# Optimization experiments

Measured on AMD Instinct MI355X. Metric: run time of the kernel, lower is better.

## Reference

```python
import jax, jax.numpy as jnp
import numpy as np

HEADS = 8
HEAD_DIM = 64
FOLD = 2   # fold_w == fold_h
PROP = 2   # proposal_w == proposal_h -> M = PROP*PROP centers
DIM = 512


def _conv1x1(x, w, b):
    # x: [B,C,H,W], w: [O,C] (1x1 conv kernel squeezed), b: [O]
    return jnp.einsum('bchw,oc->bohw', x, w) + b[None, :, None, None]


def _normalize(x):
    # F.normalize along last dim (eps-clamped L2 norm)
    n = jnp.linalg.norm(x, axis=-1, keepdims=True)
    return x / jnp.maximum(n, 1e-12)


def _fold(t, f):
    # 'b c (f1 w) (f2 h) -> (b f1 f2) c w h'
    b, c, W, H = t.shape
    return t.reshape(b, c, f, W // f, f, H // f).transpose(0, 2, 4, 1, 3, 5).reshape(b * f * f, c, W // f, H // f)


def _unfold(t, f):
    # '(b f1 f2) c w h -> b c (f1 w) (f2 h)'
    bf, c, w, h = t.shape
    b = bf // (f * f)
    return t.reshape(b, f, f, c, w, h).transpose(0, 3, 1, 4, 2, 5).reshape(b, c, f * w, f * h)


def _pool(t, p):
    # AdaptiveAvgPool2d((p,p)) when spatial dims divisible by p
    b, c, W, H = t.shape
    return t.reshape(b, c, p, W // p, p, H // p).mean(axis=(3, 5))


def reference(x, f_w, f_b, v_w, v_b, proj_w, proj_b, sim_alpha, sim_beta):
    B = x.shape[0]
    value = _conv1x1(x, v_w, v_b)
    feat = _conv1x1(x, f_w, f_b)
    # split heads: 'b (e c) w h -> (b e) c w h'
    feat = feat.reshape(B * HEADS, HEAD_DIM, feat.shape[2], feat.shape[3])
    value = value.reshape(B * HEADS, HEAD_DIM, value.shape[2], value.shape[3])
    feat = _fold(feat, FOLD)
    value = _fold(value, FOLD)
    b, c, w, h = feat.shape

    centers = _pool(feat, PROP)                                   # [b,c,p,p]
    value_centers = _pool(value, PROP).reshape(b, c, -1).transpose(0, 2, 1)  # [b,M,c]
    cflat = centers.reshape(b, c, -1).transpose(0, 2, 1)          # [b,M,c]
    M = cflat.shape[1]
    xflat = feat.reshape(b, c, -1).transpose(0, 2, 1)             # [b,N,c]

    cos = jnp.einsum('bmc,bnc->bmn', _normalize(cflat), _normalize(xflat))
    sim = jax.nn.sigmoid(sim_beta + sim_alpha * cos)              # [b,M,N]

    idx = jnp.argmax(sim, axis=1)                                 # [b,N] hard assignment
    sim_max = jnp.max(sim, axis=1)
    L_Clst = -jnp.mean(sim_max)
    mask = jax.nn.one_hot(idx, M, dtype=sim.dtype).transpose(0, 2, 1)  # [b,M,N]
    L_Sep = jnp.mean(jnp.max(sim * (1.0 - mask), axis=1))
    Cn = _normalize(cflat)
    G = jnp.einsum('bmc,bkc->bmk', Cn, Cn)
    L_Orth = jnp.mean((G - jnp.eye(M, dtype=G.dtype)) ** 2)

    sim_m = sim * mask
    vflat = value.reshape(b, c, -1).transpose(0, 2, 1)            # [b,N,c]
    # scatter_sum of values into their assigned cluster == one-hot matmul
    agg = jnp.einsum('bmn,bnc->bmc', mask, vflat)                 # [b,M,c]
    counts = mask.sum(axis=-1, keepdims=True)                     # [b,M,1]
    out = (agg + value_centers) / (counts + 1.0)                  # [b,M,c]
    # masked weighted broadcast back to points (avoids [b,M,N,c] intermediate)
    outp = jnp.einsum('bmn,bmc->bnc', sim_m, out)                 # [b,N,c]
    outp = outp.transpose(0, 2, 1).reshape(b, c, w, h)
    outp = _unfold(outp, FOLD)
    outp = outp.reshape(B, HEADS * HEAD_DIM, outp.shape[2], outp.shape[3])
    outp = _conv1x1(outp, proj_w, proj_b)
    return outp, jnp.stack([L_Orth, L_Clst, L_Sep])


def setup_inputs():
    key = jax.random.key(0)
    ks = jax.random.split(key, 4)
    E = HEADS * HEAD_DIM  # 512
    return {
        'x': jax.random.normal(ks[0], (32, DIM, 32, 32), jnp.float32),
        'f_w': jax.random.normal(ks[1], (E, DIM), jnp.float32) * 0.02,
        'f_b': jnp.zeros((E,), jnp.float32),
        'v_w': jax.random.normal(ks[2], (E, DIM), jnp.float32) * 0.02,
        'v_b': jnp.zeros((E,), jnp.float32),
        'proj_w': jax.random.normal(ks[3], (DIM, E), jnp.float32) * 0.02,
        'proj_b': jnp.zeros((DIM,), jnp.float32),
        'sim_alpha': jnp.ones((1,), jnp.float32),
        'sim_beta': jnp.zeros((1,), jnp.float32),
    }
```

## Files before the change

### kernel.cpp

```cpp
#include <hip/hip_runtime.h>


#define HW 1024

typedef _Float16 f16x8 __attribute__((ext_vector_type(8)));
typedef float f32x4 __attribute__((ext_vector_type(4)));

union H4 { uint2 u; _Float16 h[4]; };
union H8 { uint4 u; _Float16 h[8]; };
union H2 { unsigned int u; _Float16 h[2]; };
union F4 { float4 v; float f[4]; };

__device__ __forceinline__ void gld16(const _Float16* g, _Float16* l) {
    __builtin_amdgcn_global_load_lds(
        (const __attribute__((address_space(1))) void*)g,
        (__attribute__((address_space(3))) void*)l, 16, 0, 0);
}

__global__ __launch_bounds__(256) void k_wsplit(
    const float* __restrict__ fw, const float* __restrict__ vw,
    _Float16* __restrict__ fwh, _Float16* __restrict__ fwl,
    _Float16* __restrict__ vwh)
{
    const int i = (blockIdx.x * 256 + threadIdx.x) * 4;
    F4 a;
    a.v = *(const float4*)&fw[i];
    H4 h, l;
#pragma unroll
    for (int j = 0; j < 4; ++j) {
        const float s = a.f[j] * 256.f;
        h.h[j] = (_Float16)s;
        l.h[j] = (_Float16)(s - (float)h.h[j]);
    }
    *(uint2*)&fwh[i] = h.u;
    *(uint2*)&fwl[i] = l.u;
    a.v = *(const float4*)&vw[i];
#pragma unroll
    for (int j = 0; j < 4; ++j) h.h[j] = (_Float16)(a.f[j] * 256.f);
    *(uint2*)&vwh[i] = h.u;
}

__global__ __launch_bounds__(256) void k_xsplit(
    const float* __restrict__ x,
    _Float16* __restrict__ xh, _Float16* __restrict__ xl)
{
    __shared__ float tile[64][65];
    const int t = threadIdx.x;
    const int b = blockIdx.z;
    const int k0 = blockIdx.y * 64;
    const int n0 = blockIdx.x * 64;
    const float* Xb = x + (size_t)b * (512 * HW);

#pragma unroll
    for (int j = 0; j < 16; ++j) {
        const int k = j * 4 + (t >> 6);
        const int n = t & 63;
        tile[k][n] = Xb[(size_t)(k0 + k) * HW + n0 + n];
    }
    __syncthreads();
#pragma unroll
    for (int j = 0; j < 8; ++j) {
        const int n = j * 8 + (t >> 5);
        const int kp = t & 31;
        const float s0 = tile[kp * 2][n] * 256.f;
        const float s1 = tile[kp * 2 + 1][n] * 256.f;
        H2 hh, hl;
        hh.h[0] = (_Float16)s0;
        hh.h[1] = (_Float16)s1;
        hl.h[0] = (_Float16)(s0 - (float)hh.h[0]);
        hl.h[1] = (_Float16)(s1 - (float)hh.h[1]);
        const size_t o = ((size_t)b * 1024 + n0 + n) * 512 + k0 + kp * 2;
        *(unsigned int*)&xh[o] = hh.u;
        *(unsigned int*)&xl[o] = hl.u;
    }
}

__global__ __launch_bounds__(256) void k_feat(
    const _Float16* __restrict__ fwh, const _Float16* __restrict__ fwl,
    const float* __restrict__ bias,
    const _Float16* __restrict__ xh, const _Float16* __restrict__ xl,
    float* __restrict__ feat_T, float* __restrict__ centers_f)
{
    __shared__ _Float16 Ah[128 * 32], Al[128 * 32], Bh[128 * 32], Bl[128 * 32];
    __shared__ float pool_lds[2][128][4];
    const int t = threadIdx.x, lane = t & 63, wv = t >> 6;
    const int b = blockIdx.z, o0 = blockIdx.y * 128, p0 = blockIdx.x * 128;
    const int wr = wv >> 1, wc = wv & 1;

    f32x4 acc[4][4];
#pragma unroll
    for (int i = 0; i < 4; ++i)
#pragma unroll
        for (int j = 0; j < 4; ++j) acc[i][j] = (f32x4){0.f, 0.f, 0.f, 0.f};

    const _Float16* ash = fwh + (size_t)(o0 + wv * 32 + (lane >> 2)) * 512 + (lane & 3) * 8;
    const _Float16* asl = fwl + (size_t)(o0 + wv * 32 + (lane >> 2)) * 512 + (lane & 3) * 8;
    const size_t brow = (size_t)b * 1024 + p0 + wv * 32 + (lane >> 2);
    const _Float16* bsh = xh + brow * 512 + (lane & 3) * 8;
    const _Float16* bsl = xl + brow * 512 + (lane & 3) * 8;

    for (int kb = 0; kb < 16; ++kb) {
        const int k0 = kb * 32;
        __syncthreads();
#pragma unroll
        for (int j = 0; j < 2; ++j) {
            gld16(ash + (size_t)(j * 16) * 512 + k0, &Ah[(wv * 32 + j * 16) * 32]);
            gld16(asl + (size_t)(j * 16) * 512 + k0, &Al[(wv * 32 + j * 16) * 32]);
            gld16(bsh + (size_t)(j * 16) * 512 + k0, &Bh[(wv * 32 + j * 16) * 32]);
            gld16(bsl + (size_t)(j * 16) * 512 + k0, &Bl[(wv * 32 + j * 16) * 32]);
        }
        __syncthreads();
        f16x8 ah[4], al[4], bh[4], bl[4];
#pragma unroll
        for (int i = 0; i < 4; ++i) {
            const int ao = (wr * 64 + i * 16 + (lane & 15)) * 32 + (lane >> 4) * 8;
            const int bo = (wc * 64 + i * 16 + (lane & 15)) * 32 + (lane >> 4) * 8;
            ah[i] = *(f16x8*)&Ah[ao];
            al[i] = *(f16x8*)&Al[ao];
            bh[i] = *(f16x8*)&Bh[bo];
            bl[i] = *(f16x8*)&Bl[bo];
        }
#pragma unroll
        for (int mi = 0; mi < 4; ++mi)
#pragma unroll
            for (int nj = 0; nj < 4; ++nj) {
                acc[mi][nj] = __builtin_amdgcn_mfma_f32_16x16x32_f16(ah[mi], bh[nj], acc[mi][nj], 0, 0, 0);
                acc[mi][nj] = __builtin_amdgcn_mfma_f32_16x16x32_f16(ah[mi], bl[nj], acc[mi][nj], 0, 0, 0);
                acc[mi][nj] = __builtin_amdgcn_mfma_f32_16x16x32_f16(al[mi], bh[nj], acc[mi][nj], 0, 0, 0);
            }
    }

    const int pj = (lane >> 3) & 1;
    float ps[16][2];
#pragma unroll
    for (int mi = 0; mi < 4; ++mi) {
        const int obase = o0 + wr * 64 + mi * 16 + (lane >> 4) * 4;
        F4 bs4;
        bs4.v = *(const float4*)&bias[obase];
#pragma unroll
        for (int r = 0; r < 4; ++r) { ps[mi * 4 + r][0] = 0.f; ps[mi * 4 + r][1] = 0.f; }
#pragma unroll
        for (int nj = 0; nj < 4; ++nj) {
            const int p = p0 + wc * 64 + nj * 16 + (lane & 15);
            F4 vv;
#pragma unroll
            for (int r = 0; r < 4; ++r) {
                vv.f[r] = acc[mi][nj][r] * (1.f / 65536.f) + bs4.f[r];
                ps[mi * 4 + r][nj & 1] += vv.f[r];
            }
            *(float4*)&feat_T[((size_t)b * 1024 + p) * 512 + obase] = vv.v;
        }
    }
#pragma unroll
    for (int q = 0; q < 16; ++q)
#pragma unroll
        for (int f2s = 0; f2s < 2; ++f2s) {
            ps[q][f2s] += __shfl_xor(ps[q][f2s], 1);
            ps[q][f2s] += __shfl_xor(ps[q][f2s], 2);
            ps[q][f2s] += __shfl_xor(ps[q][f2s], 4);
        }
    if ((lane & 7) == 0) {
#pragma unroll
        for (int mi = 0; mi < 4; ++mi)
#pragma unroll
            for (int r = 0; r < 4; ++r) {
                const int ol = wr * 64 + mi * 16 + (lane >> 4) * 4 + r;
                pool_lds[wc][ol][0 * 2 + pj] = ps[mi * 4 + r][0];
                pool_lds[wc][ol][1 * 2 + pj] = ps[mi * 4 + r][1];
            }
    }
    __syncthreads();
#pragma unroll
    for (int u = 0; u < 2; ++u) {
        const int idx = u * 256 + t;
        const int g = idx >> 7, o = idx & 127;
        centers_f[(((size_t)b * 8 + blockIdx.x) * 4 + g) * 512 + o0 + o] =
            pool_lds[0][o][g] + pool_lds[1][o][g];
    }
}

__global__ __launch_bounds__(256) void k_value(
    const _Float16* __restrict__ vwh, const float* __restrict__ bias,
    const _Float16* __restrict__ xh,
    _Float16* __restrict__ value_T, float* __restrict__ centers_v)
{
    __shared__ _Float16 Ah[128 * 32], Bh[128 * 32];
    __shared__ float pool_lds[2][128][4];
    const int t = threadIdx.x, lane = t & 63, wv = t >> 6;
    const int b = blockIdx.z, o0 = blockIdx.y * 128, p0 = blockIdx.x * 128;
    const int wr = wv >> 1, wc = wv & 1;

    f32x4 acc[4][4];
#pragma unroll
    for (int i = 0; i < 4; ++i)
#pragma unroll
        for (int j = 0; j < 4; ++j) acc[i][j] = (f32x4){0.f, 0.f, 0.f, 0.f};

    const _Float16* ash = vwh + (size_t)(o0 + wv * 32 + (lane >> 2)) * 512 + (lane & 3) * 8;
    const _Float16* bsh = xh + ((size_t)b * 1024 + p0 + wv * 32 + (lane >> 2)) * 512 + (lane & 3) * 8;

    for (int kb = 0; kb < 16; ++kb) {
        const int k0 = kb * 32;
        __syncthreads();
#pragma unroll
        for (int j = 0; j < 2; ++j) {
            gld16(ash + (size_t)(j * 16) * 512 + k0, &Ah[(wv * 32 + j * 16) * 32]);
            gld16(bsh + (size_t)(j * 16) * 512 + k0, &Bh[(wv * 32 + j * 16) * 32]);
        }
        __syncthreads();
        f16x8 ah[4], bh[4];
#pragma unroll
        for (int i = 0; i < 4; ++i) {
            ah[i] = *(f16x8*)&Ah[(wr * 64 + i * 16 + (lane & 15)) * 32 + (lane >> 4) * 8];
            bh[i] = *(f16x8*)&Bh[(wc * 64 + i * 16 + (lane & 15)) * 32 + (lane >> 4) * 8];
        }
#pragma unroll
        for (int mi = 0; mi < 4; ++mi)
#pragma unroll
            for (int nj = 0; nj < 4; ++nj)
                acc[mi][nj] = __builtin_amdgcn_mfma_f32_16x16x32_f16(ah[mi], bh[nj], acc[mi][nj], 0, 0, 0);
    }

    const int pj = (lane >> 3) & 1;
    float ps[16][2];
#pragma unroll
    for (int mi = 0; mi < 4; ++mi) {
        const int obase = o0 + wr * 64 + mi * 16 + (lane >> 4) * 4;
        F4 bs4;
        bs4.v = *(const float4*)&bias[obase];
#pragma unroll
        for (int r = 0; r < 4; ++r) { ps[mi * 4 + r][0] = 0.f; ps[mi * 4 + r][1] = 0.f; }
#pragma unroll
        for (int nj = 0; nj < 4; ++nj) {
            const int p = p0 + wc * 64 + nj * 16 + (lane & 15);
            H4 hv;
#pragma unroll
            for (int r = 0; r < 4; ++r) {
                const float v = acc[mi][nj][r] * (1.f / 65536.f) + bs4.f[r];
                ps[mi * 4 + r][nj & 1] += v;
                hv.h[r] = (_Float16)v;
            }
            *(uint2*)&value_T[((size_t)b * 1024 + p) * 512 + obase] = hv.u;
        }
    }
#pragma unroll
    for (int q = 0; q < 16; ++q)
#pragma unroll
        for (int f2s = 0; f2s < 2; ++f2s) {
            ps[q][f2s] += __shfl_xor(ps[q][f2s], 1);
            ps[q][f2s] += __shfl_xor(ps[q][f2s], 2);
            ps[q][f2s] += __shfl_xor(ps[q][f2s], 4);
        }
    if ((lane & 7) == 0) {
#pragma unroll
        for (int mi = 0; mi < 4; ++mi)
#pragma unroll
            for (int r = 0; r < 4; ++r) {
                const int ol = wr * 64 + mi * 16 + (lane >> 4) * 4 + r;
                pool_lds[wc][ol][0 * 2 + pj] = ps[mi * 4 + r][0];
                pool_lds[wc][ol][1 * 2 + pj] = ps[mi * 4 + r][1];
            }
    }
    __syncthreads();
#pragma unroll
    for (int u = 0; u < 2; ++u) {
        const int idx = u * 256 + t;
        const int g = idx >> 7, o = idx & 127;
        centers_v[(((size_t)b * 8 + blockIdx.x) * 4 + g) * 512 + o0 + o] =
            pool_lds[0][o][g] + pool_lds[1][o][g];
    }
}

__global__ __launch_bounds__(256) void k_cluster(
    const float* __restrict__ feat_T, const _Float16* __restrict__ value_T,
    const float* __restrict__ centers_f, const float* __restrict__ centers_v,
    const float* __restrict__ alpha_p, const float* __restrict__ beta_p,
    _Float16* __restrict__ outpT, float* __restrict__ part)
{
    __shared__ _Float16 vbuf[256 * 64];
    __shared__ float cnl[4][64];
    __shared__ float vcl[4][64];
    __shared__ float obuf[4][68];
    __shared__ int   sidx[256];
    __shared__ float sbest[256];
    __shared__ float scrt[4][4][64];
    __shared__ int   cntw[4][4];
    __shared__ float red[8];
    __shared__ float gsc[16];

    const int t = threadIdx.x, lane = t & 63, wv = t >> 6;
    const int bp = blockIdx.x;
    const int f2 = bp & 1, f1 = (bp >> 1) & 1, head = (bp >> 2) & 7, b = bp >> 5;

    const int m = wv, cc = lane;
    const int pi = m >> 1, pj = m & 1, g = f2 * 2 + pj;
    const int pt = 4 * f1 + 2 * pi;
    {
        const float* cf = centers_f + (((size_t)b * 8 + pt) * 4 + g) * 512 + head * 64 + cc;
        const float c = (cf[0] + cf[4 * 512]) * (1.f / 64.f);
        float ss = c * c;
#pragma unroll
        for (int off = 32; off > 0; off >>= 1) ss += __shfl_xor(ss, off);
        const float inv = 1.f / fmaxf(sqrtf(ss), 1e-12f);
        cnl[m][cc] = c * inv;
        const float* cv = centers_v + (((size_t)b * 8 + pt) * 4 + g) * 512 + head * 64 + cc;
        vcl[m][cc] = (cv[0] + cv[4 * 512]) * (1.f / 64.f);
    }
    __syncthreads();

    if (t < 16) {
        const int gm = t >> 2, gk = t & 3;
        float gg = 0.f;
        for (int c = 0; c < 64; ++c) gg += cnl[gm][c] * cnl[gk][c];
        const float d = gg - (gm == gk ? 1.f : 0.f);
        gsc[t] = d * d;
    }

    const float alpha = alpha_p[0], beta = beta_p[0];
    const int n = t;
    const int pg = (f1 * 16 + (n >> 4)) * 32 + f2 * 16 + (n & 15);
    const float* fp = feat_T + ((size_t)b * 1024 + pg) * 512 + head * 64;
    float ssf = 0.f, d0 = 0.f, d1 = 0.f, d2 = 0.f, d3 = 0.f;
#pragma unroll
    for (int c4 = 0; c4 < 16; ++c4) {
        F4 fv;
        fv.v = *(const float4*)&fp[c4 * 4];
        const float4 c0 = *(const float4*)&cnl[0][c4 * 4];
        const float4 c1 = *(const float4*)&cnl[1][c4 * 4];
        const float4 c2 = *(const float4*)&cnl[2][c4 * 4];
        const float4 c3 = *(const float4*)&cnl[3][c4 * 4];
        ssf += fv.f[0]*fv.f[0] + fv.f[1]*fv.f[1] + fv.f[2]*fv.f[2] + fv.f[3]*fv.f[3];
        d0 += fv.f[0]*c0.x + fv.f[1]*c0.y + fv.f[2]*c0.z + fv.f[3]*c0.w;
        d1 += fv.f[0]*c1.x + fv.f[1]*c1.y + fv.f[2]*c1.z + fv.f[3]*c1.w;
        d2 += fv.f[0]*c2.x + fv.f[1]*c2.y + fv.f[2]*c2.z + fv.f[3]*c2.w;
        d3 += fv.f[0]*c3.x + fv.f[1]*c3.y + fv.f[2]*c3.z + fv.f[3]*c3.w;
    }
    const float invf = 1.f / fmaxf(sqrtf(ssf), 1e-12f);
    float simv[4];
    simv[0] = d0 * invf;
    simv[1] = d1 * invf;
    simv[2] = d2 * invf;
    simv[3] = d3 * invf;
#pragma unroll
    for (int mm = 0; mm < 4; ++mm)
        simv[mm] = 1.f / (1.f + expf(-(beta + alpha * simv[mm])));
    float best = simv[0], second = -1.f;
    int idx = 0;
#pragma unroll
    for (int mm = 1; mm < 4; ++mm) {
        if (simv[mm] > best) { second = best; best = simv[mm]; idx = mm; }
        else second = fmaxf(second, simv[mm]);
    }
    sidx[n] = idx;
    sbest[n] = best;

    const _Float16* vp = value_T + ((size_t)b * 1024 + pg) * 512 + head * 64;
#pragma unroll
    for (int j = 0; j < 8; ++j) {
        const uint4 v = *(const uint4*)&vp[j * 8];
        *(uint4*)&vbuf[n * 64 + ((j * 8) ^ ((n & 7) << 3))] = v;
    }

    float bsum = best, s2sum = second;
#pragma unroll
    for (int off = 32; off > 0; off >>= 1) {
        bsum += __shfl_xor(bsum, off);
        s2sum += __shfl_xor(s2sum, off);
    }
    if (lane == 0) { red[wv] = bsum; red[4 + wv] = s2sum; }
    __syncthreads();
    if (t == 0) {
        part[bp]        = gsc[0] + gsc[1] + gsc[2] + gsc[3] + gsc[4] + gsc[5] + gsc[6] + gsc[7]
                        + gsc[8] + gsc[9] + gsc[10] + gsc[11] + gsc[12] + gsc[13] + gsc[14] + gsc[15];
        part[1024 + bp] = red[0] + red[1] + red[2] + red[3];
        part[2048 + bp] = red[4] + red[5] + red[6] + red[7];
    }

    {
        float ag0 = 0.f, ag1 = 0.f, ag2 = 0.f, ag3 = 0.f;
        int c0i = 0, c1i = 0, c2i = 0, c3i = 0;
        for (int j = 0; j < 64; ++j) {
            const int nn = wv * 64 + j;
            const int id = sidx[nn];
            const float v = (float)vbuf[nn * 64 + (cc ^ ((nn & 7) << 3))];
            ag0 += (id == 0) ? v : 0.f;  c0i += (id == 0);
            ag1 += (id == 1) ? v : 0.f;  c1i += (id == 1);
            ag2 += (id == 2) ? v : 0.f;  c2i += (id == 2);
            ag3 += (id == 3) ? v : 0.f;  c3i += (id == 3);
        }
        scrt[wv][0][cc] = ag0;
        scrt[wv][1][cc] = ag1;
        scrt[wv][2][cc] = ag2;
        scrt[wv][3][cc] = ag3;
        if (lane == 0) {
            cntw[wv][0] = c0i; cntw[wv][1] = c1i;
            cntw[wv][2] = c2i; cntw[wv][3] = c3i;
        }
    }
    __syncthreads();

    {
        const float a = scrt[0][m][cc] + scrt[1][m][cc] + scrt[2][m][cc] + scrt[3][m][cc];
        const int c = cntw[0][m] + cntw[1][m] + cntw[2][m] + cntw[3][m];
        obuf[m][cc] = (a + vcl[m][cc]) / (float)(c + 1);
    }
    __syncthreads();

    const int cch = (t & 3) * 16;
#pragma unroll
    for (int r = 0; r < 4; ++r) {
        const int nn = r * 64 + (t >> 2);
        const int id = sidx[nn];
        const float bs = sbest[nn];
        const int p = (f1 * 16 + (nn >> 4)) * 32 + f2 * 16 + (nn & 15);
        _Float16* dst = outpT + (((size_t)b * 8 + head) * 1024 + p) * 64 + cch;
        const float4 oa = *(const float4*)&obuf[id][cch];
        const float4 ob = *(const float4*)&obuf[id][cch + 4];
        const float4 oc = *(const float4*)&obuf[id][cch + 8];
        const float4 od = *(const float4*)&obuf[id][cch + 12];
        H8 w0, w1;
        w0.h[0] = (_Float16)(bs * oa.x); w0.h[1] = (_Float16)(bs * oa.y);
        w0.h[2] = (_Float16)(bs * oa.z); w0.h[3] = (_Float16)(bs * oa.w);
        w0.h[4] = (_Float16)(bs * ob.x); w0.h[5] = (_Float16)(bs * ob.y);
        w0.h[6] = (_Float16)(bs * ob.z); w0.h[7] = (_Float16)(bs * ob.w);
        w1.h[0] = (_Float16)(bs * oc.x); w1.h[1] = (_Float16)(bs * oc.y);
        w1.h[2] = (_Float16)(bs * oc.z); w1.h[3] = (_Float16)(bs * oc.w);
        w1.h[4] = (_Float16)(bs * od.x); w1.h[5] = (_Float16)(bs * od.y);
        w1.h[6] = (_Float16)(bs * od.z); w1.h[7] = (_Float16)(bs * od.w);
        *(uint4*)dst = w0.u;
        *(uint4*)(dst + 8) = w1.u;
    }
}

__global__ __launch_bounds__(256) void k_proj(
    const float* __restrict__ w, const float* __restrict__ bias,
    const _Float16* __restrict__ outpT,
    const float* __restrict__ part,
    float* __restrict__ dout)
{
    __shared__ _Float16 Ah[128 * 32], Bh[128 * 32];
    __shared__ float fin[12];
    const int t = threadIdx.x, lane = t & 63, wv = t >> 6;

    if (blockIdx.x == 0 && blockIdx.y == 0 && blockIdx.z == 0) {
        float so = part[t] + part[t + 256] + part[t + 512] + part[t + 768];
        float sc = part[1024 + t] + part[1280 + t] + part[1536 + t] + part[1792 + t];
        float sp = part[2048 + t] + part[2304 + t] + part[2560 + t] + part[2816 + t];
#pragma unroll
        for (int off = 32; off > 0; off >>= 1) {
            so += __shfl_xor(so, off);
            sc += __shfl_xor(sc, off);
            sp += __shfl_xor(sp, off);
        }
        if (lane == 0) { fin[wv] = so; fin[4 + wv] = sc; fin[8 + wv] = sp; }
        __syncthreads();
        if (t == 0) {
            dout[16777216]     = (fin[0] + fin[1] + fin[2] + fin[3]) / 16384.f;
            dout[16777216 + 1] = -(fin[4] + fin[5] + fin[6] + fin[7]) / 262144.f;
            dout[16777216 + 2] = (fin[8] + fin[9] + fin[10] + fin[11]) / 262144.f;
        }
        __syncthreads();
    }

    const int b = blockIdx.z, o0 = blockIdx.y * 128, p0 = blockIdx.x * 128;
    const int wr = wv >> 1, wc = wv & 1;

    f32x4 acc[4][4];
#pragma unroll
    for (int i = 0; i < 4; ++i)
#pragma unroll
        for (int j = 0; j < 4; ++j) acc[i][j] = (f32x4){0.f, 0.f, 0.f, 0.f};

    const int srow = p0 + wv * 32 + (lane >> 2);
    const int scol = (lane & 3) * 8;

    for (int kb = 0; kb < 16; ++kb) {
        const int k0 = kb * 32;
        F4 av[4];
#pragma unroll
        for (int j = 0; j < 4; ++j) {
            const int idx = j * 256 + t, row = idx >> 3, q = idx & 7;
            av[j].v = *(const float4*)&w[(size_t)(o0 + row) * 512 + k0 + q * 4];
        }
        __syncthreads();
#pragma unroll
        for (int j = 0; j < 4; ++j) {
            const int idx = j * 256 + t, row = idx >> 3, q = idx & 7;
            H4 hh;
#pragma unroll
            for (int i = 0; i < 4; ++i) hh.h[i] = (_Float16)(av[j].f[i] * 256.f);
            *(uint2*)&Ah[row * 32 + q * 4] = hh.u;
        }
        const _Float16* bsrc = outpT + (((size_t)b * 8 + (kb >> 1)) * 1024 + srow) * 64
                               + (kb & 1) * 32 + scol;
        gld16(bsrc,            &Bh[(wv * 32) * 32]);
        gld16(bsrc + 16 * 64,  &Bh[(wv * 32 + 16) * 32]);
        __syncthreads();
        f16x8 ah[4], bh[4];
#pragma unroll
        for (int i = 0; i < 4; ++i) {
            ah[i] = *(f16x8*)&Ah[(wr * 64 + i * 16 + (lane & 15)) * 32 + (lane >> 4) * 8];
            bh[i] = *(f16x8*)&Bh[(wc * 64 + i * 16 + (lane & 15)) * 32 + (lane >> 4) * 8];
        }
#pragma unroll
        for (int mi = 0; mi < 4; ++mi)
#pragma unroll
            for (int nj = 0; nj < 4; ++nj)
                acc[mi][nj] = __builtin_amdgcn_mfma_f32_16x16x32_f16(ah[mi], bh[nj], acc[mi][nj], 0, 0, 0);
    }
#pragma unroll
    for (int mi = 0; mi < 4; ++mi)
#pragma unroll
        for (int r = 0; r < 4; ++r) {
            const int o = o0 + wr * 64 + mi * 16 + (lane >> 4) * 4 + r;
            const float bs = bias[o];
#pragma unroll
            for (int nj = 0; nj < 4; ++nj) {
                const int p = p0 + wc * 64 + nj * 16 + (lane & 15);
                dout[((size_t)b * 512 + o) * HW + p] = acc[mi][nj][r] * (1.f / 256.f) + bs;
            }
        }
}

extern "C" void kernel_launch(void* const* d_in, const int* in_sizes, int n_in,
                              void* d_out, int out_size, void* d_ws, size_t ws_size,
                              hipStream_t stream)
{
    const float* x   = (const float*)d_in[0];
    const float* f_w = (const float*)d_in[1];
    const float* f_b = (const float*)d_in[2];
    const float* v_w = (const float*)d_in[3];
    const float* v_b = (const float*)d_in[4];
    const float* p_w = (const float*)d_in[5];
    const float* p_b = (const float*)d_in[6];
    const float* s_a = (const float*)d_in[7];
    const float* s_b = (const float*)d_in[8];
    float* out = (float*)d_out;

    char* ws = (char*)d_ws;
    float*     feat_T  = (float*)ws;
    _Float16*  xh      = (_Float16*)(ws + (size_t)64 * 1024 * 1024);
    _Float16*  xl      = (_Float16*)(ws + (size_t)96 * 1024 * 1024);
    _Float16*  outpT   = xh;
    _Float16*  value_T = xl;
    float*     part    = (float*)(ws + (size_t)128 * 1024 * 1024);

    _Float16* fwh       = (_Float16*)out;
    _Float16* fwl       = (_Float16*)(out + 131072);
    _Float16* vwh       = (_Float16*)(out + 262144);
    float*    centers_f = out + 393216;
    float*    centers_v = out + 917504;

    k_wsplit <<<dim3(256), 256, 0, stream>>>(f_w, v_w, fwh, fwl, vwh);
    k_xsplit <<<dim3(16, 8, 32), 256, 0, stream>>>(x, xh, xl);
    k_feat   <<<dim3(8, 4, 32), 256, 0, stream>>>(fwh, fwl, f_b, xh, xl, feat_T, centers_f);
    k_value  <<<dim3(8, 4, 32), 256, 0, stream>>>(vwh, v_b, xh, value_T, centers_v);
    k_cluster<<<dim3(1024), 256, 0, stream>>>(feat_T, value_T, centers_f, centers_v,
                                              s_a, s_b, outpT, part);
    k_proj   <<<dim3(8, 4, 32), 256, 0, stream>>>(p_w, p_b, outpT, part, out);
}
```

Before: 202.0 us.

## Double-buffer LDS tiles and XOR-swizzle layout in the three GEMM kernels

Converts the feat, value and projection GEMM main loops to double-buffered LDS, so the global-to-LDS loads for the next K-tile are issued while MFMAs run on the current tile. This also cuts the loop to one barrier per iteration. The LDS layout is XOR-swizzled on both the write and read sides to reduce bank conflicts on the f16x8 fragment reads. The cost is twice the shared memory, which may lower occupancy, and more complex index math.

```diff
diff --git a/kernel.cpp b/kernel.cpp
--- a/kernel.cpp
+++ b/kernel.cpp
@@ -81,7 +81,7 @@
     const _Float16* __restrict__ xh, const _Float16* __restrict__ xl,
     float* __restrict__ feat_T, float* __restrict__ centers_f)
 {
-    __shared__ _Float16 Ah[128 * 32], Al[128 * 32], Bh[128 * 32], Bl[128 * 32];
+    __shared__ _Float16 Ah[2][4096], Al[2][4096], Bh[2][4096], Bl[2][4096];
     __shared__ float pool_lds[2][128][4];
     const int t = threadIdx.x, lane = t & 63, wv = t >> 6;
     const int b = blockIdx.z, o0 = blockIdx.y * 128, p0 = blockIdx.x * 128;
@@ -93,42 +93,53 @@
 #pragma unroll
         for (int j = 0; j < 4; ++j) acc[i][j] = (f32x4){0.f, 0.f, 0.f, 0.f};
 
-    const _Float16* ash = fwh + (size_t)(o0 + wv * 32 + (lane >> 2)) * 512 + (lane & 3) * 8;
-    const _Float16* asl = fwl + (size_t)(o0 + wv * 32 + (lane >> 2)) * 512 + (lane & 3) * 8;
+    const int gslot = ((lane & 3) ^ ((lane >> 3) & 3)) * 8;
+    const _Float16* ash = fwh + (size_t)(o0 + wv * 32 + (lane >> 2)) * 512 + gslot;
+    const _Float16* asl = fwl + (size_t)(o0 + wv * 32 + (lane >> 2)) * 512 + gslot;
     const size_t brow = (size_t)b * 1024 + p0 + wv * 32 + (lane >> 2);
-    const _Float16* bsh = xh + brow * 512 + (lane & 3) * 8;
-    const _Float16* bsl = xl + brow * 512 + (lane & 3) * 8;
-
+    const _Float16* bsh = xh + brow * 512 + gslot;
+    const _Float16* bsl = xl + brow * 512 + gslot;
+
+#define STAGE_F(d, k0)                                              \
+    {                                                               \
+        gld16(ash + (k0),        &Ah[(d)][(wv * 32) * 32]);         \
+        gld16(ash + (k0) + 8192, &Ah[(d)][(wv * 32 + 16) * 32]);    \
+        gld16(asl + (k0),        &Al[(d)][(wv * 32) * 32]);         \
+        gld16(asl + (k0) + 8192, &Al[(d)][(wv * 32 + 16) * 32]);    \
+        gld16(bsh + (k0),        &Bh[(d)][(wv * 32) * 32]);         \
+        gld16(bsh + (k0) + 8192, &Bh[(d)][(wv * 32 + 16) * 32]);    \
+        gld16(bsl + (k0),        &Bl[(d)][(wv * 32) * 32]);         \
+        gld16(bsl + (k0) + 8192, &Bl[(d)][(wv * 32 + 16) * 32]);    \
+    }
+
+    STAGE_F(0, 0);
+    __syncthreads();
+    const int slA = ((lane >> 4) ^ ((lane >> 1) & 3)) * 8;
+    int cur = 0;
     for (int kb = 0; kb < 16; ++kb) {
-        const int k0 = kb * 32;
+        if (kb < 15) STAGE_F(cur ^ 1, (kb + 1) * 32);
+        f16x8 ah4[4], al4[4], bh4[4], bl4[4];
+#pragma unroll
+        for (int i = 0; i < 4; ++i) {
+            const int ao = (wr * 64 + i * 16 + (lane & 15)) * 32 + slA;
+            const int bo = (wc * 64 + i * 16 + (lane & 15)) * 32 + slA;
+            ah4[i] = *(f16x8*)&Ah[cur][ao];
+            al4[i] = *(f16x8*)&Al[cur][ao];
+            bh4[i] = *(f16x8*)&Bh[cur][bo];
+            bl4[i] = *(f16x8*)&Bl[cur][bo];
+        }
+#pragma unroll
+        for (int mi = 0; mi < 4; ++mi)
+#pragma unroll
+            for (int nj = 0; nj < 4; ++nj) {
+                acc[mi][nj] = __builtin_amdgcn_mfma_f32_16x16x32_f16(ah4[mi], bh4[nj], acc[mi][nj], 0, 0, 0);
+                acc[mi][nj] = __builtin_amdgcn_mfma_f32_16x16x32_f16(ah4[mi], bl4[nj], acc[mi][nj], 0, 0, 0);
+                acc[mi][nj] = __builtin_amdgcn_mfma_f32_16x16x32_f16(al4[mi], bh4[nj], acc[mi][nj], 0, 0, 0);
+            }
         __syncthreads();
-#pragma unroll
-        for (int j = 0; j < 2; ++j) {
-            gld16(ash + (size_t)(j * 16) * 512 + k0, &Ah[(wv * 32 + j * 16) * 32]);
-            gld16(asl + (size_t)(j * 16) * 512 + k0, &Al[(wv * 32 + j * 16) * 32]);
-            gld16(bsh + (size_t)(j * 16) * 512 + k0, &Bh[(wv * 32 + j * 16) * 32]);
-            gld16(bsl + (size_t)(j * 16) * 512 + k0, &Bl[(wv * 32 + j * 16) * 32]);
-        }
-        __syncthreads();
-        f16x8 ah[4], al[4], bh[4], bl[4];
-#pragma unroll
-        for (int i = 0; i < 4; ++i) {
-            const int ao = (wr * 64 + i * 16 + (lane & 15)) * 32 + (lane >> 4) * 8;
-            const int bo = (wc * 64 + i * 16 + (lane & 15)) * 32 + (lane >> 4) * 8;
-            ah[i] = *(f16x8*)&Ah[ao];
-            al[i] = *(f16x8*)&Al[ao];
-            bh[i] = *(f16x8*)&Bh[bo];
-            bl[i] = *(f16x8*)&Bl[bo];
-        }
-#pragma unroll
-        for (int mi = 0; mi < 4; ++mi)
-#pragma unroll
-            for (int nj = 0; nj < 4; ++nj) {
-                acc[mi][nj] = __builtin_amdgcn_mfma_f32_16x16x32_f16(ah[mi], bh[nj], acc[mi][nj], 0, 0, 0);
-                acc[mi][nj] = __builtin_amdgcn_mfma_f32_16x16x32_f16(ah[mi], bl[nj], acc[mi][nj], 0, 0, 0);
-                acc[mi][nj] = __builtin_amdgcn_mfma_f32_16x16x32_f16(al[mi], bh[nj], acc[mi][nj], 0, 0, 0);
-            }
-    }
+        cur ^= 1;
+    }
+#undef STAGE_F
 
     const int pj = (lane >> 3) & 1;
     float ps[16][2];
@@ -184,7 +195,7 @@
     const _Float16* __restrict__ xh,
     _Float16* __restrict__ value_T, float* __restrict__ centers_v)
 {
-    __shared__ _Float16 Ah[128 * 32], Bh[128 * 32];
+    __shared__ _Float16 Ah[2][4096], Bh[2][4096];
     __shared__ float pool_lds[2][128][4];
     const int t = threadIdx.x, lane = t & 63, wv = t >> 6;
     const int b = blockIdx.z, o0 = blockIdx.y * 128, p0 = blockIdx.x * 128;
@@ -196,30 +207,39 @@
 #pragma unroll
         for (int j = 0; j < 4; ++j) acc[i][j] = (f32x4){0.f, 0.f, 0.f, 0.f};
 
-    const _Float16* ash = vwh + (size_t)(o0 + wv * 32 + (lane >> 2)) * 512 + (lane & 3) * 8;
-    const _Float16* bsh = xh + ((size_t)b * 1024 + p0 + wv * 32 + (lane >> 2)) * 512 + (lane & 3) * 8;
-
+    const int gslot = ((lane & 3) ^ ((lane >> 3) & 3)) * 8;
+    const _Float16* ash = vwh + (size_t)(o0 + wv * 32 + (lane >> 2)) * 512 + gslot;
+    const _Float16* bsh = xh + ((size_t)b * 1024 + p0 + wv * 32 + (lane >> 2)) * 512 + gslot;
+
+#define STAGE_V(d, k0)                                              \
+    {                                                               \
+        gld16(ash + (k0),        &Ah[(d)][(wv * 32) * 32]);         \
+        gld16(ash + (k0) + 8192, &Ah[(d)][(wv * 32 + 16) * 32]);    \
+        gld16(bsh + (k0),        &Bh[(d)][(wv * 32) * 32]);         \
+        gld16(bsh + (k0) + 8192, &Bh[(d)][(wv * 32 + 16) * 32]);    \
+    }
+
+    STAGE_V(0, 0);
+    __syncthreads();
+    const int slA = ((lane >> 4) ^ ((lane >> 1) & 3)) * 8;
+    int cur = 0;
     for (int kb = 0; kb < 16; ++kb) {
-        const int k0 = kb * 32;
+        if (kb < 15) STAGE_V(cur ^ 1, (kb + 1) * 32);
+        f16x8 ah4[4], bh4[4];
+#pragma unroll
+        for (int i = 0; i < 4; ++i) {
+            ah4[i] = *(f16x8*)&Ah[cur][(wr * 64 + i * 16 + (lane & 15)) * 32 + slA];
+            bh4[i] = *(f16x8*)&Bh[cur][(wc * 64 + i * 16 + (lane & 15)) * 32 + slA];
+        }
+#pragma unroll
+        for (int mi = 0; mi < 4; ++mi)
+#pragma unroll
+            for (int nj = 0; nj < 4; ++nj)
+                acc[mi][nj] = __builtin_amdgcn_mfma_f32_16x16x32_f16(ah4[mi], bh4[nj], acc[mi][nj], 0, 0, 0);
         __syncthreads();
-#pragma unroll
-        for (int j = 0; j < 2; ++j) {
-            gld16(ash + (size_t)(j * 16) * 512 + k0, &Ah[(wv * 32 + j * 16) * 32]);
-            gld16(bsh + (size_t)(j * 16) * 512 + k0, &Bh[(wv * 32 + j * 16) * 32]);
-        }
-        __syncthreads();
-        f16x8 ah[4], bh[4];
-#pragma unroll
-        for (int i = 0; i < 4; ++i) {
-            ah[i] = *(f16x8*)&Ah[(wr * 64 + i * 16 + (lane & 15)) * 32 + (lane >> 4) * 8];
-            bh[i] = *(f16x8*)&Bh[(wc * 64 + i * 16 + (lane & 15)) * 32 + (lane >> 4) * 8];
-        }
-#pragma unroll
-        for (int mi = 0; mi < 4; ++mi)
-#pragma unroll
-            for (int nj = 0; nj < 4; ++nj)
-                acc[mi][nj] = __builtin_amdgcn_mfma_f32_16x16x32_f16(ah[mi], bh[nj], acc[mi][nj], 0, 0, 0);
-    }
+        cur ^= 1;
+    }
+#undef STAGE_V
 
     const int pj = (lane >> 3) & 1;
     float ps[16][2];
@@ -438,7 +458,7 @@
     const float* __restrict__ part,
     float* __restrict__ dout)
 {
-    __shared__ _Float16 Ah[128 * 32], Bh[128 * 32];
+    __shared__ _Float16 As[2][4096], Bs[2][4096];
     __shared__ float fin[12];
     const int t = threadIdx.x, lane = t & 63, wv = t >> 6;
 
@@ -471,43 +491,67 @@
 #pragma unroll
         for (int j = 0; j < 4; ++j) acc[i][j] = (f32x4){0.f, 0.f, 0.f, 0.f};
 
+    const int gslot = ((lane & 3) ^ ((lane >> 3) & 3)) * 8;
     const int srow = p0 + wv * 32 + (lane >> 2);
-    const int scol = (lane & 3) * 8;
-
+    const int arow_l = t >> 3;
+    const int aq = t & 7;
+    const int aqs = aq ^ (((t >> 4) & 3) << 1);
+
+    F4 av[4];
+#define LOADA(k0)                                                        \
+    {                                                                    \
+        _Pragma("unroll")                                                \
+        for (int j = 0; j < 4; ++j)                                      \
+            av[j].v = *(const float4*)&w[(size_t)(o0 + j * 32 + arow_l) * 512 + (k0) + aq * 4]; \
+    }
+#define WRITEA(d)                                                        \
+    {                                                                    \
+        _Pragma("unroll")                                                \
+        for (int j = 0; j < 4; ++j) {                                    \
+            H4 hh;                                                       \
+            _Pragma("unroll")                                            \
+            for (int i = 0; i < 4; ++i) hh.h[i] = (_Float16)(av[j].f[i] * 256.f); \
+            *(uint2*)&As[(d)][(j * 32 + arow_l) * 32 + aqs * 4] = hh.u;  \
+        }                                                                \
+    }
+#define STAGEB(d, kb)                                                    \
+    {                                                                    \
+        const _Float16* bsrc = outpT + (((size_t)b * 8 + ((kb) >> 1)) * 1024 + srow) * 64 \
+                               + ((kb) & 1) * 32 + gslot;                \
+        gld16(bsrc,        &Bs[(d)][(wv * 32) * 32]);                    \
+        gld16(bsrc + 1024, &Bs[(d)][(wv * 32 + 16) * 32]);               \
+    }
+
+    LOADA(0);
+    STAGEB(0, 0);
+    WRITEA(0);
+    __syncthreads();
+    const int slA = ((lane >> 4) ^ ((lane >> 1) & 3)) * 8;
+    int cur = 0;
     for (int kb = 0; kb < 16; ++kb) {
-        const int k0 = kb * 32;
-        F4 av[4];
-#pragma unroll
-        for (int j = 0; j < 4; ++j) {
-            const int idx = j * 256 + t, row = idx >> 3, q = idx & 7;
-            av[j].v = *(const float4*)&w[(size_t)(o0 + row) * 512 + k0 + q * 4];
-        }
+        if (kb < 15) {
+            LOADA((kb + 1) * 32);
+            STAGEB(cur ^ 1, kb + 1);
+        }
+        f16x8 ah4[4], bh4[4];
+#pragma unroll
+        for (int i = 0; i < 4; ++i) {
+            ah4[i] = *(f16x8*)&As[cur][(wr * 64 + i * 16 + (lane & 15)) * 32 + slA];
+            bh4[i] = *(f16x8*)&Bs[cur][(wc * 64 + i * 16 + (lane & 15)) * 32 + slA];
+        }
+#pragma unroll
+        for (int mi = 0; mi < 4; ++mi)
+#pragma unroll
+            for (int nj = 0; nj < 4; ++nj)
+                acc[mi][nj] = __builtin_amdgcn_mfma_f32_16x16x32_f16(ah4[mi], bh4[nj], acc[mi][nj], 0, 0, 0);
+        if (kb < 15) WRITEA(cur ^ 1);
         __syncthreads();
-#pragma unroll
-        for (int j = 0; j < 4; ++j) {
-            const int idx = j * 256 + t, row = idx >> 3, q = idx & 7;
-            H4 hh;
-#pragma unroll
-            for (int i = 0; i < 4; ++i) hh.h[i] = (_Float16)(av[j].f[i] * 256.f);
-            *(uint2*)&Ah[row * 32 + q * 4] = hh.u;
-        }
-        const _Float16* bsrc = outpT + (((size_t)b * 8 + (kb >> 1)) * 1024 + srow) * 64
-                               + (kb & 1) * 32 + scol;
-        gld16(bsrc,            &Bh[(wv * 32) * 32]);
-        gld16(bsrc + 16 * 64,  &Bh[(wv * 32 + 16) * 32]);
-        __syncthreads();
-        f16x8 ah[4], bh[4];
-#pragma unroll
-        for (int i = 0; i < 4; ++i) {
-            ah[i] = *(f16x8*)&Ah[(wr * 64 + i * 16 + (lane & 15)) * 32 + (lane >> 4) * 8];
-            bh[i] = *(f16x8*)&Bh[(wc * 64 + i * 16 + (lane & 15)) * 32 + (lane >> 4) * 8];
-        }
-#pragma unroll
-        for (int mi = 0; mi < 4; ++mi)
-#pragma unroll
-            for (int nj = 0; nj < 4; ++nj)
-                acc[mi][nj] = __builtin_amdgcn_mfma_f32_16x16x32_f16(ah[mi], bh[nj], acc[mi][nj], 0, 0, 0);
-    }
+        cur ^= 1;
+    }
+#undef LOADA
+#undef WRITEA
+#undef STAGEB
+
 #pragma unroll
     for (int mi = 0; mi < 4; ++mi)
 #pragma unroll
```

After: 203.8 us. No clear change (+0.9%).
